# Kernel optimization log

Hardware: AMD Instinct MI355X
Metric: run time of the kernel (lower is better)

Reference implementation:

```python
import jax, jax.numpy as jnp
import numpy as np

# static config (matches init_kwargs / chosen grid)
T, H, W = 8, 32, 32          # video token grid
WT, WH, WW = 4, 8, 8         # swin window
HEADS, HD = 16, 128
DIM = HEADS * HD             # 2048
LT = 256                     # text length
EPS = 1e-6
NT, NH, NW_ = T // WT, H // WH, W // WW
NWIN = NT * NH * NW_
WLEN = WT * WH * WW


def rmsnorm(x, g):
    # x: [..., HD], g: [HD]
    var = jnp.mean(x * x, axis=-1, keepdims=True)
    return x * jax.lax.rsqrt(var + EPS) * g


def setup_inputs() -> dict:
    key = jax.random.key(0)
    ks = jax.random.split(key, 8)
    s = 0.02
    Lv = T * H * W
    return {
        'vid': jax.random.normal(ks[0], (Lv, DIM), jnp.float32),
        'txt': jax.random.normal(ks[1], (LT, DIM), jnp.float32),
        'Wqkv_v': jax.random.normal(ks[2], (DIM, 3 * DIM), jnp.float32) * s,
        'bqkv_v': jnp.zeros((3 * DIM,), jnp.float32),
        'Wqkv_t': jax.random.normal(ks[3], (DIM, 3 * DIM), jnp.float32) * s,
        'bqkv_t': jnp.zeros((3 * DIM,), jnp.float32),
        'Wo_v': jax.random.normal(ks[4], (DIM, DIM), jnp.float32) * s,
        'bo_v': jnp.zeros((DIM,), jnp.float32),
        'Wo_t': jax.random.normal(ks[5], (DIM, DIM), jnp.float32) * s,
        'bo_t': jnp.zeros((DIM,), jnp.float32),
        'gq_v': jnp.ones((HD,), jnp.float32),
        'gk_v': jnp.ones((HD,), jnp.float32),
        'gq_t': jnp.ones((HD,), jnp.float32),
        'gk_t': jnp.ones((HD,), jnp.float32),
    }


def _forward(vid, txt, Wqkv_v, bqkv_v, Wqkv_t, bqkv_t, Wo_v, bo_v, Wo_t, bo_t,
             gq_v, gk_v, gq_t, gk_t):
    # per-modality QKV projections
    vqkv = vid @ Wqkv_v + bqkv_v                      # [Lv, 3*DIM]
    tqkv = txt @ Wqkv_t + bqkv_t                      # [LT, 3*DIM]
    # swin window partition: [T,H,W,C] -> [nWin, WLEN, 3, h, d]
    x = vqkv.reshape(NT, WT, NH, WH, NW_, WW, 3 * DIM)
    x = x.transpose(0, 2, 4, 1, 3, 5, 6).reshape(NWIN, WLEN, 3, HEADS, HD)
    vq, vk, vv = x[:, :, 0], x[:, :, 1], x[:, :, 2]
    t = tqkv.reshape(LT, 3, HEADS, HD)
    tq, tk, tv = t[:, 0], t[:, 1], t[:, 2]
    # QK norm (per-head RMSNorm with affine)
    vq, vk = rmsnorm(vq, gq_v), rmsnorm(vk, gk_v)
    tq, tk = rmsnorm(tq, gq_t), rmsnorm(tk, gk_t)
    # concat full text to every window (repeat_concat_idx)
    bt = lambda a: jnp.broadcast_to(a[None], (NWIN,) + a.shape)
    q = jnp.concatenate([vq, bt(tq)], axis=1)          # [nWin, S, h, d]
    k = jnp.concatenate([vk, bt(tk)], axis=1)
    v = jnp.concatenate([vv, bt(tv)], axis=1)
    # attention within each window (flash-varlen equivalent, equal lengths)
    scale = 1.0 / np.sqrt(HD).astype(np.float32)
    scores = jnp.einsum('nqhd,nkhd->nhqk', q, k) * scale
    p = jax.nn.softmax(scores, axis=-1)
    o = jnp.einsum('nhqk,nkhd->nqhd', p, v)            # [nWin, S, h, d]
    vo = o[:, :WLEN].reshape(NWIN, WLEN, DIM)
    to = o[:, WLEN:].mean(axis=0).reshape(LT, DIM)     # un-repeat text: mean over windows
    # window reverse -> flat [Lv, DIM]
    vo = vo.reshape(NT, NH, NW_, WT, WH, WW, DIM)
    vo = vo.transpose(0, 3, 1, 4, 2, 5, 6).reshape(T * H * W, DIM)
    return (vo @ Wo_v + bo_v, to @ Wo_t + bo_t)


def reference(vid, txt, Wqkv_v, bqkv_v, Wqkv_t, bqkv_t, Wo_v, bo_v, Wo_t, bo_t,
              gq_v, gk_v, gq_t, gk_t):
    return _forward(vid, txt, Wqkv_v, bqkv_v, Wqkv_t, bqkv_t, Wo_v, bo_v,
                    Wo_t, bo_t, gq_v, gk_v, gq_t, gk_t)
```

## Files before the change

### kernel.cpp

```cpp
#include <hip/hip_runtime.h>

typedef unsigned short u16;
typedef unsigned int   u32;
typedef __attribute__((ext_vector_type(8))) short short8;
typedef __attribute__((ext_vector_type(4))) float f32x4;

__device__ __forceinline__ u16 f2bf(float f) {
  union { float f; u32 u; } v; v.f = f;
  u32 r = v.u + 0x7fffu + ((v.u >> 16) & 1u);
  return (u16)(r >> 16);
}
__device__ __forceinline__ float bf2f(u32 bits) {
  union { u32 u; float f; } v; v.u = bits << 16; return v.f;
}
__device__ __forceinline__ void gl_lds16(const u16* g, u16* l) {
  __builtin_amdgcn_global_load_lds(
      (const __attribute__((address_space(1))) void*)g,
      (__attribute__((address_space(3))) void*)l, 16, 0, 0);
}

static constexpr int DIM  = 2048;
static constexpr int NQKV = 6144;

__global__ __launch_bounds__(256) void conv_f32_bf16(const float* __restrict__ in,
                                                     u16* __restrict__ out, int n4) {
  int id = blockIdx.x * 256 + threadIdx.x;
  if (id >= n4) return;
  float4 v = ((const float4*)in)[id];
  u32 lo = (u32)f2bf(v.x) | ((u32)f2bf(v.y) << 16);
  u32 hi = (u32)f2bf(v.z) | ((u32)f2bf(v.w) << 16);
  ((uint2*)out)[id] = make_uint2(lo, hi);
}

__global__ void tconv_kernel(const float* __restrict__ W, u16* __restrict__ Wt, int K, int N) {
  __shared__ float t[32][33];
  int tx = threadIdx.x, ty = threadIdx.y;
  int n0 = blockIdx.x * 32, k0 = blockIdx.y * 32;
  #pragma unroll
  for (int i = 0; i < 4; ++i)
    t[ty + i*8][tx] = W[(size_t)(k0 + ty + i*8) * N + n0 + tx];
  __syncthreads();
  #pragma unroll
  for (int i = 0; i < 4; ++i)
    Wt[(size_t)(n0 + ty + i*8) * K + k0 + tx] = f2bf(t[tx][ty + i*8]);
}

__global__ __launch_bounds__(256) void rms_kernel(u16* __restrict__ x,
                                                  const float* __restrict__ g, int nrows) {
  int w = threadIdx.x >> 6, lane = threadIdx.x & 63;
  int rid = blockIdx.x * 4 + w;
  if (rid >= nrows) return;
  u32* row = (u32*)x + (size_t)rid * 64;
  u32 u = row[lane];
  float f0 = bf2f(u & 0xffffu), f1 = bf2f(u >> 16);
  float s = f0*f0 + f1*f1;
  #pragma unroll
  for (int off = 1; off <= 32; off <<= 1) s += __shfl_xor(s, off);
  float r = rsqrtf(s * (1.0f/128.0f) + 1e-6f);
  float g0 = g[lane*2], g1 = g[lane*2+1];
  row[lane] = (u32)f2bf(f0*r*g0) | ((u32)f2bf(f1*r*g1) << 16);
}

__global__ __launch_bounds__(256)
void vtrans_kernel(const u16* __restrict__ src, u16* __restrict__ dst) {
  __shared__ u16 t[64][130];
  int nh = blockIdx.x, k0 = blockIdx.y * 64;
  const u16* s = src + ((size_t)nh*256 + k0)*128;
  u16* d = dst + (size_t)nh*128*256 + k0;
  int tid = threadIdx.x;
  #pragma unroll
  for (int it = 0; it < 4; ++it) {
    int c = tid + it*256;
    int row = c >> 4, ch = c & 15;
    short8 v = *(const short8*)(s + row*128 + ch*8);
    u32* dst32 = (u32*)&t[row][ch*8];
    const u32* v32 = (const u32*)&v;
    dst32[0] = v32[0]; dst32[1] = v32[1]; dst32[2] = v32[2]; dst32[3] = v32[3];
  }
  __syncthreads();
  #pragma unroll
  for (int it = 0; it < 4; ++it) {
    int c = tid + it*256;
    int dr = c >> 3, kg = c & 7;
    short8 v;
    #pragma unroll
    for (int j = 0; j < 8; ++j) v[j] = (short)t[kg*8+j][dr];
    *(short8*)(d + (size_t)dr*256 + kg*8) = v;
  }
}

template<int EPI>
__global__ __launch_bounds__(512, 2)
void gemm256(const u16* __restrict__ A, const u16* __restrict__ Bt,
             const float* __restrict__ bias,
             u16* __restrict__ o0, u16* __restrict__ o1, u16* __restrict__ o2,
             float* __restrict__ of, int ldo, int M, int N, int K)
{
  __shared__ __align__(16) u16 As[4][256*32];
  __shared__ __align__(16) u16 Bs[4][256*32];
  const int NT = K >> 5;
  int tid = threadIdx.x, lane = tid & 63, w = tid >> 6;
  int l15 = lane & 15, l4 = lane >> 4;
  int wm = w >> 2, wn = w & 3;

  int nbx = gridDim.x;
  int nwg = nbx * gridDim.y;
  int bid = blockIdx.y * nbx + blockIdx.x;
  int cpx = nwg >> 3;
  int swz = (bid & 7) * cpx + (bid >> 3);
  int n0 = (swz % nbx) * 256, m0 = (swz / nbx) * 256;

  int srow = tid >> 2, skc = (tid & 3) ^ ((tid >> 3) & 3);
  const u16* aS = A  + (size_t)(m0 + srow) * K + skc * 8;
  const u16* bS = Bt + (size_t)(n0 + srow) * K + skc * 8;
  const size_t halfStride = 128 * (size_t)K;
  const int ldsBase = w * 512;

  #define STAGE_A(slot, tt, half) \
    gl_lds16(aS + (size_t)(tt)*32 + (half)*halfStride, &As[slot][(half)*4096 + ldsBase])
  #define STAGE_B(slot, tt, half) \
    gl_lds16(bS + (size_t)(tt)*32 + (half)*halfStride, &Bs[slot][(half)*4096 + ldsBase])

  #pragma unroll
  for (int pt = 0; pt < 3; ++pt) {
    STAGE_A(pt, pt, 0); STAGE_A(pt, pt, 1);
    STAGE_B(pt, pt, 0); STAGE_B(pt, pt, 1);
  }

  f32x4 acc[8][4] = {};

  for (int t = 0; t < NT; ++t) {
    if (t < NT - 2)       asm volatile("s_waitcnt vmcnt(8)" ::: "memory");
    else if (t == NT - 2) asm volatile("s_waitcnt vmcnt(4)" ::: "memory");
    else                  asm volatile("s_waitcnt vmcnt(0)" ::: "memory");
    __builtin_amdgcn_s_barrier();
    asm volatile("" ::: "memory");

    const u16* ab = As[t & 3];
    const u16* bb = Bs[t & 3];
    bool st = (t + 3 < NT);
    int slot = (t + 3) & 3;

    short8 bf_[4];
    #pragma unroll
    for (int j = 0; j < 4; ++j) {
      int rb = wn*64 + j*16 + l15;
      bf_[j] = *(const short8*)((const char*)bb + rb*64 + ((l4 ^ ((rb>>1)&3))*16));
    }

    short8 af[4];
    #pragma unroll
    for (int i = 0; i < 4; ++i) {
      int ra = wm*128 + i*16 + l15;
      af[i] = *(const short8*)((const char*)ab + ra*64 + ((l4 ^ ((ra>>1)&3))*16));
    }
    if (st) { STAGE_A(slot, t+3, 0); STAGE_A(slot, t+3, 1); }
    __builtin_amdgcn_s_setprio(1);
    #pragma unroll
    for (int i = 0; i < 4; ++i)
      #pragma unroll
      for (int j = 0; j < 4; ++j)
        acc[i][j] = __builtin_amdgcn_mfma_f32_16x16x32_bf16(af[i], bf_[j], acc[i][j], 0, 0, 0);
    __builtin_amdgcn_s_setprio(0);

    #pragma unroll
    for (int i = 0; i < 4; ++i) {
      int ra = wm*128 + 64 + i*16 + l15;
      af[i] = *(const short8*)((const char*)ab + ra*64 + ((l4 ^ ((ra>>1)&3))*16));
    }
    if (st) { STAGE_B(slot, t+3, 0); STAGE_B(slot, t+3, 1); }
    __builtin_amdgcn_s_setprio(1);
    #pragma unroll
    for (int i = 0; i < 4; ++i)
      #pragma unroll
      for (int j = 0; j < 4; ++j)
        acc[4+i][j] = __builtin_amdgcn_mfma_f32_16x16x32_bf16(af[i], bf_[j], acc[4+i][j], 0, 0, 0);
    __builtin_amdgcn_s_setprio(0);
  }
  #undef STAGE_A
  #undef STAGE_B

  #pragma unroll
  for (int i = 0; i < 8; ++i)
    #pragma unroll
    for (int j = 0; j < 4; ++j)
      #pragma unroll
      for (int r = 0; r < 4; ++r) {
        int m = m0 + wm*128 + i*16 + l4*4 + r;
        int n = n0 + wn*64  + j*16 + l15;
        float v = acc[i][j][r] + bias[n];
        if (EPI == 0) {
          int which = n >> 11, head = (n >> 7) & 15, d = n & 127;
          int t = m >> 10, hh = (m >> 5) & 31, ww = m & 31;
          int win = ((t>>2)<<4) + ((hh>>3)<<2) + (ww>>3);
          int p   = ((t&3)<<6) + ((hh&7)<<3) + (ww&7);
          u16* dst = which == 0 ? o0 : (which == 1 ? o1 : o2);
          dst[((size_t)(win*16 + head)*256 + p)*128 + d] = f2bf(v);
        } else {
          of[(size_t)m * ldo + n] = v;
        }
      }
}

template<int EPI>
__global__ __launch_bounds__(256)
void gemm128(const u16* __restrict__ A, const u16* __restrict__ Bt,
             const float* __restrict__ bias,
             u16* __restrict__ o0, u16* __restrict__ o1, u16* __restrict__ o2,
             float* __restrict__ of, int ldo, int M, int N, int K)
{
  __shared__ __align__(16) u16 As[128*32];
  __shared__ __align__(16) u16 Bs[128*32];
  int tid = threadIdx.x, lane = tid & 63, w = tid >> 6;
  int l15 = lane & 15, l4 = lane >> 4;
  int m0 = blockIdx.y * 128, n0 = blockIdx.x * 128;
  int wr = (w >> 1) * 64, wc = (w & 1) * 64;
  f32x4 acc[4][4] = {};

  int o0b = (w    )*1024 + lane*16;
  int o1b = (w + 4)*1024 + lane*16;
  int r0 = o0b >> 6, c0 = ((o0b >> 4) & 3) ^ ((r0 >> 1) & 3);
  int r1 = o1b >> 6, c1 = ((o1b >> 4) & 3) ^ ((r1 >> 1) & 3);
  const u16* a0 = A  + (size_t)(m0 + r0)*K + c0*8;
  const u16* a1 = A  + (size_t)(m0 + r1)*K + c1*8;
  const u16* b0 = Bt + (size_t)(n0 + r0)*K + c0*8;
  const u16* b1 = Bt + (size_t)(n0 + r1)*K + c1*8;
  u16* dA0 = As + (w    )*512;
  u16* dA1 = As + (w + 4)*512;
  u16* dB0 = Bs + (w    )*512;
  u16* dB1 = Bs + (w + 4)*512;

  for (int k0 = 0; k0 < K; k0 += 32) {
    gl_lds16(a0 + k0, dA0);
    gl_lds16(a1 + k0, dA1);
    gl_lds16(b0 + k0, dB0);
    gl_lds16(b1 + k0, dB1);
    __syncthreads();
    short8 af[4], bfr[4];
    #pragma unroll
    for (int t = 0; t < 4; ++t) {
      int ra = wr + t*16 + l15;
      af[t]  = *(const short8*)((const char*)As + ra*64 + ((l4 ^ ((ra>>1)&3))*16));
      int rb = wc + t*16 + l15;
      bfr[t] = *(const short8*)((const char*)Bs + rb*64 + ((l4 ^ ((rb>>1)&3))*16));
    }
    #pragma unroll
    for (int i = 0; i < 4; ++i)
      #pragma unroll
      for (int j = 0; j < 4; ++j)
        acc[i][j] = __builtin_amdgcn_mfma_f32_16x16x32_bf16(af[i], bfr[j], acc[i][j], 0, 0, 0);
    __syncthreads();
  }

  #pragma unroll
  for (int i = 0; i < 4; ++i)
    #pragma unroll
    for (int j = 0; j < 4; ++j)
      #pragma unroll
      for (int r = 0; r < 4; ++r) {
        int m = m0 + wr + i*16 + l4*4 + r;
        int n = n0 + wc + j*16 + l15;
        float v = acc[i][j][r] + bias[n];
        if (EPI == 1) {
          int which = n >> 11, head = (n >> 7) & 15, d = n & 127;
          u16* dst = which == 0 ? o0 : (which == 1 ? o1 : o2);
          dst[((size_t)head*256 + m)*128 + d] = f2bf(v);
        } else {
          of[(size_t)m * ldo + n] = v;
        }
      }
}

__global__ __launch_bounds__(512)
void attn_kernel(const u16* __restrict__ vq, const u16* __restrict__ vk, const u16* __restrict__ vv,
                 const u16* __restrict__ tq, const u16* __restrict__ tk, const u16* __restrict__ tv,
                 const float* __restrict__ gq_v, const float* __restrict__ gq_t,
                 u16* __restrict__ vo, float* __restrict__ to_acc)
{
  __shared__ __align__(16) u16 Ks[64*128];
  __shared__ __align__(16) u16 Vt[128*64];
  __shared__ __align__(16) u16 Ps[8][16*80];
  int tid = threadIdx.x, lane = tid & 63, w = tid >> 6;
  int l15 = lane & 15, l4 = lane >> 4;
  int nh_ = blockIdx.x;
  int h = nh_ & 15;
  int n = nh_ >> 4;
  int qt = blockIdx.y * 128 + w * 16;

  const u16* Qb; const float* gq;
  if (qt < 256) { Qb = vq + ((size_t)nh_*256 + qt)*128; gq = gq_v; }
  else          { Qb = tq + ((size_t)h  *256 + (qt-256))*128; gq = gq_t; }
  short8 qf[4];
  float qv[4][8];
  float ss = 0.f;
  #pragma unroll
  for (int dt = 0; dt < 4; ++dt) {
    qf[dt] = *(const short8*)(Qb + l15*128 + l4*8 + dt*32);
    #pragma unroll
    for (int j = 0; j < 8; ++j) {
      float f = bf2f((u16)qf[dt][j]);
      qv[dt][j] = f; ss += f*f;
    }
  }
  ss += __shfl_xor(ss, 16); ss += __shfl_xor(ss, 32);
  float rr = rsqrtf(ss * (1.0f/128.0f) + 1e-6f);
  #pragma unroll
  for (int dt = 0; dt < 4; ++dt) {
    float4 g0 = *(const float4*)(gq + l4*8 + dt*32);
    float4 g1 = *(const float4*)(gq + l4*8 + dt*32 + 4);
    qf[dt][0] = (short)f2bf(qv[dt][0]*rr*g0.x); qf[dt][1] = (short)f2bf(qv[dt][1]*rr*g0.y);
    qf[dt][2] = (short)f2bf(qv[dt][2]*rr*g0.z); qf[dt][3] = (short)f2bf(qv[dt][3]*rr*g0.w);
    qf[dt][4] = (short)f2bf(qv[dt][4]*rr*g1.x); qf[dt][5] = (short)f2bf(qv[dt][5]*rr*g1.y);
    qf[dt][6] = (short)f2bf(qv[dt][6]*rr*g1.z); qf[dt][7] = (short)f2bf(qv[dt][7]*rr*g1.w);
  }

  int oK0 = w*1024 + lane*16, oK1 = oK0 + 8192;
  int kr0 = oK0 >> 8, kc0 = ((oK0 >> 4) & 15) ^ (kr0 & 7);
  int kr1 = oK1 >> 8, kc1 = ((oK1 >> 4) & 15) ^ (kr1 & 7);
  int vd0 = oK0 >> 7, vc0 = ((oK0 >> 4) & 7) ^ (vd0 & 7);
  int vd1 = oK1 >> 7, vc1 = ((oK1 >> 4) & 7) ^ (vd1 & 7);
  u16* KD0 = Ks + (w*1024)/2;  u16* KD1 = Ks + (w*1024 + 8192)/2;
  u16* VD0 = Vt + (w*1024)/2;  u16* VD1 = Vt + (w*1024 + 8192)/2;

  f32x4 o_[8] = {};
  float m_run[4] = {-1e30f,-1e30f,-1e30f,-1e30f};
  float l_run[4] = {0.f,0.f,0.f,0.f};
  const float scale = 0.08838834764831845f;

  for (int c = 0; c < 8; ++c) {
    int kb = c * 64;
    const u16* Kc; const u16* Vb; int vkb;
    if (kb < 256) { Kc = vk + ((size_t)nh_*256 + kb)*128; Vb = vv + (size_t)nh_*128*256; vkb = kb; }
    else          { Kc = tk + ((size_t)h  *256 + (kb-256))*128; Vb = tv + (size_t)h*128*256; vkb = kb - 256; }
    gl_lds16(Kc + kr0*128 + kc0*8, KD0);
    gl_lds16(Kc + kr1*128 + kc1*8, KD1);
    gl_lds16(Vb + (size_t)vd0*256 + vkb + vc0*8, VD0);
    gl_lds16(Vb + (size_t)vd1*256 + vkb + vc1*8, VD1);
    __syncthreads();

    f32x4 s4[4];
    #pragma unroll
    for (int kt = 0; kt < 4; ++kt) {
      f32x4 sa = {0.f,0.f,0.f,0.f};
      int key = kt*16 + l15;
      #pragma unroll
      for (int dt = 0; dt < 4; ++dt) {
        int c16b = l4 + dt*4;
        short8 kf = *(const short8*)((const char*)Ks + key*256 + (((c16b ^ (key&7)))*16));
        sa = __builtin_amdgcn_mfma_f32_16x16x32_bf16(qf[dt], kf, sa, 0, 0, 0);
      }
      s4[kt] = sa;
    }

    float f_[4];
    #pragma unroll
    for (int r = 0; r < 4; ++r) {
      float mx = fmaxf(fmaxf(s4[0][r], s4[1][r]), fmaxf(s4[2][r], s4[3][r])) * scale;
      #pragma unroll
      for (int off = 1; off <= 8; off <<= 1) mx = fmaxf(mx, __shfl_xor(mx, off));
      float nm = fmaxf(m_run[r], mx);
      f_[r] = __expf(m_run[r] - nm);
      m_run[r] = nm;
    }
    float p[4][4];
    #pragma unroll
    for (int kt = 0; kt < 4; ++kt)
      #pragma unroll
      for (int r = 0; r < 4; ++r)
        p[kt][r] = __expf(s4[kt][r]*scale - m_run[r]);
    #pragma unroll
    for (int r = 0; r < 4; ++r) {
      float sum = p[0][r] + p[1][r] + p[2][r] + p[3][r];
      #pragma unroll
      for (int off = 1; off <= 8; off <<= 1) sum += __shfl_xor(sum, off);
      l_run[r] = l_run[r]*f_[r] + sum;
    }
    #pragma unroll
    for (int dt = 0; dt < 8; ++dt) {
      f32x4 t = o_[dt];
      t[0]*=f_[0]; t[1]*=f_[1]; t[2]*=f_[2]; t[3]*=f_[3];
      o_[dt] = t;
    }

    u16* pb = Ps[w];
    #pragma unroll
    for (int kt = 0; kt < 4; ++kt)
      #pragma unroll
      for (int r = 0; r < 4; ++r)
        pb[(l4*4 + r)*80 + kt*16 + l15] = f2bf(p[kt][r]);
    __syncthreads();
    #pragma unroll
    for (int ks = 0; ks < 2; ++ks) {
      short8 pa = *(const short8*)((const char*)pb + l15*160 + ks*64 + l4*16);
      #pragma unroll
      for (int dt = 0; dt < 8; ++dt) {
        int d = dt*16 + l15;
        short8 vf = *(const short8*)((const char*)Vt + d*128 + (((ks*4 + l4) ^ (d&7))<<4));
        o_[dt] = __builtin_amdgcn_mfma_f32_16x16x32_bf16(pa, vf, o_[dt], 0, 0, 0);
      }
    }
    __syncthreads();
  }

  float inv[4];
  #pragma unroll
  for (int r = 0; r < 4; ++r) inv[r] = 1.0f / l_run[r];
  int nt = n >> 4, nh2 = (n >> 2) & 3, nw = n & 3;
  #pragma unroll
  for (int dt = 0; dt < 8; ++dt) {
    int d = dt*16 + l15;
    int col = h*128 + d;
    #pragma unroll
    for (int r = 0; r < 4; ++r) {
      float val = o_[dt][r] * inv[r];
      int q = qt + l4*4 + r;
      if (q < 256) {
        int wt = q >> 6, wh = (q >> 3) & 7, ww = q & 7;
        int rg = ((nt*4 + wt)*32 + (nh2*8 + wh))*32 + (nw*8 + ww);
        vo[(size_t)rg*2048 + col] = f2bf(val);
      } else {
        atomicAdd(to_acc + (size_t)(q - 256)*2048 + col, val * (1.0f/32.0f));
      }
    }
  }
}

extern "C" void kernel_launch(void* const* d_in, const int* in_sizes, int n_in,
                              void* d_out, int out_size, void* d_ws, size_t ws_size,
                              hipStream_t stream) {
  const float* vid    = (const float*)d_in[0];
  const float* txt    = (const float*)d_in[1];
  const float* Wqkv_v = (const float*)d_in[2];
  const float* bqkv_v = (const float*)d_in[3];
  const float* Wqkv_t = (const float*)d_in[4];
  const float* bqkv_t = (const float*)d_in[5];
  const float* Wo_v   = (const float*)d_in[6];
  const float* bo_v   = (const float*)d_in[7];
  const float* Wo_t   = (const float*)d_in[8];
  const float* bo_t   = (const float*)d_in[9];
  const float* gq_v   = (const float*)d_in[10];
  const float* gk_v   = (const float*)d_in[11];
  const float* gq_t   = (const float*)d_in[12];
  const float* gk_t   = (const float*)d_in[13];
  float* out = (float*)d_out;

  char* p = (char*)d_ws;
  u16* vid_bf   = (u16*)p;  p += 8192ull*2048*2;
  u16* txt_bf   = (u16*)p;  p += 256ull*2048*2;
  u16* Wqkv_v_t = (u16*)p;  p += 6144ull*2048*2;
  u16* Wqkv_t_t = (u16*)p;  p += 6144ull*2048*2;
  u16* Wo_v_t   = (u16*)p;  p += 2048ull*2048*2;
  u16* Wo_t_t   = (u16*)p;  p += 2048ull*2048*2;
  u16* vq_w     = (u16*)p;  p += 32ull*16*256*128*2;
  u16* vk_w     = (u16*)p;  p += 32ull*16*256*128*2;
  u16* vv_w     = (u16*)p;  p += 32ull*16*256*128*2;
  u16* tq_w     = (u16*)p;  p += 16ull*256*128*2;
  u16* tk_w     = (u16*)p;  p += 16ull*256*128*2;
  u16* tv_w     = (u16*)p;  p += 16ull*256*128*2;
  u16* vo_pre   = (u16*)p;  p += 8192ull*2048*2;
  float* to_pre = (float*)p; p += 256ull*2048*4;
  u16* to_bf    = (u16*)p;  p += 256ull*2048*2;
  u16* vvT = vid_bf;
  u16* tvT = vid_bf + 512ull*128*256;

  hipMemsetAsync(to_pre, 0, 256ull*2048*4, stream);

  conv_f32_bf16<<<dim3(16384), dim3(256), 0, stream>>>(vid, vid_bf, 8192*2048/4);
  conv_f32_bf16<<<dim3(512),   dim3(256), 0, stream>>>(txt, txt_bf, 256*2048/4);
  tconv_kernel<<<dim3(192,64), dim3(32,8), 0, stream>>>(Wqkv_v, Wqkv_v_t, 2048, 6144);
  tconv_kernel<<<dim3(192,64), dim3(32,8), 0, stream>>>(Wqkv_t, Wqkv_t_t, 2048, 6144);
  tconv_kernel<<<dim3(64,64),  dim3(32,8), 0, stream>>>(Wo_v,   Wo_v_t,   2048, 2048);
  tconv_kernel<<<dim3(64,64),  dim3(32,8), 0, stream>>>(Wo_t,   Wo_t_t,   2048, 2048);

  gemm256<0><<<dim3(24,32), dim3(512), 0, stream>>>(vid_bf, Wqkv_v_t, bqkv_v,
      vq_w, vk_w, vv_w, nullptr, 0, 8192, NQKV, DIM);
  gemm128<1><<<dim3(48,2),  dim3(256), 0, stream>>>(txt_bf, Wqkv_t_t, bqkv_t,
      tq_w, tk_w, tv_w, nullptr, 0, 256, NQKV, DIM);

  vtrans_kernel<<<dim3(512,4), dim3(256), 0, stream>>>(vv_w, vvT);
  vtrans_kernel<<<dim3(16,4),  dim3(256), 0, stream>>>(tv_w, tvT);

  rms_kernel<<<dim3(32768), dim3(256), 0, stream>>>(vk_w, gk_v, 32*16*256);
  rms_kernel<<<dim3(1024),  dim3(256), 0, stream>>>(tk_w, gk_t, 16*256);

  attn_kernel<<<dim3(512,4), dim3(512), 0, stream>>>(vq_w, vk_w, vvT, tq_w, tk_w, tvT,
                                                     gq_v, gq_t, vo_pre, to_pre);

  conv_f32_bf16<<<dim3(512), dim3(256), 0, stream>>>(to_pre, to_bf, 256*2048/4);

  gemm256<2><<<dim3(8,32), dim3(512), 0, stream>>>(vo_pre, Wo_v_t, bo_v,
      nullptr, nullptr, nullptr, out, 2048, 8192, 2048, 2048);
  gemm128<2><<<dim3(16,2), dim3(256), 0, stream>>>(to_bf, Wo_t_t, bo_t,
      nullptr, nullptr, nullptr, out + 16777216, 2048, 256, 2048, 2048);
}
```

Before: 641.8 us.

## Restructure GEMM barrier schedule and remap attention blocks with priority hints

```diff
diff --git a/kernel.cpp b/kernel.cpp
--- a/kernel.cpp
+++ b/kernel.cpp
@@ -126,35 +126,32 @@
     STAGE_A(pt, pt, 0); STAGE_A(pt, pt, 1);
     STAGE_B(pt, pt, 0); STAGE_B(pt, pt, 1);
   }
+  asm volatile("s_waitcnt vmcnt(8)" ::: "memory");
+  __builtin_amdgcn_s_barrier();
 
   f32x4 acc[8][4] = {};
 
   for (int t = 0; t < NT; ++t) {
-    if (t < NT - 2)       asm volatile("s_waitcnt vmcnt(8)" ::: "memory");
-    else if (t == NT - 2) asm volatile("s_waitcnt vmcnt(4)" ::: "memory");
-    else                  asm volatile("s_waitcnt vmcnt(0)" ::: "memory");
-    __builtin_amdgcn_s_barrier();
-    asm volatile("" ::: "memory");
-
     const u16* ab = As[t & 3];
     const u16* bb = Bs[t & 3];
     bool st = (t + 3 < NT);
     int slot = (t + 3) & 3;
 
-    short8 bf_[4];
+    short8 bf_[4], af[4];
     #pragma unroll
     for (int j = 0; j < 4; ++j) {
       int rb = wn*64 + j*16 + l15;
       bf_[j] = *(const short8*)((const char*)bb + rb*64 + ((l4 ^ ((rb>>1)&3))*16));
     }
-
-    short8 af[4];
     #pragma unroll
     for (int i = 0; i < 4; ++i) {
       int ra = wm*128 + i*16 + l15;
       af[i] = *(const short8*)((const char*)ab + ra*64 + ((l4 ^ ((ra>>1)&3))*16));
     }
     if (st) { STAGE_A(slot, t+3, 0); STAGE_A(slot, t+3, 1); }
+    __builtin_amdgcn_s_barrier();
+    asm volatile("s_waitcnt lgkmcnt(0)" ::: "memory");
+    __builtin_amdgcn_sched_barrier(0);
     __builtin_amdgcn_s_setprio(1);
     #pragma unroll
     for (int i = 0; i < 4; ++i)
@@ -162,6 +159,7 @@
       for (int j = 0; j < 4; ++j)
         acc[i][j] = __builtin_amdgcn_mfma_f32_16x16x32_bf16(af[i], bf_[j], acc[i][j], 0, 0, 0);
     __builtin_amdgcn_s_setprio(0);
+    __builtin_amdgcn_s_barrier();
 
     #pragma unroll
     for (int i = 0; i < 4; ++i) {
@@ -169,6 +167,9 @@
       af[i] = *(const short8*)((const char*)ab + ra*64 + ((l4 ^ ((ra>>1)&3))*16));
     }
     if (st) { STAGE_B(slot, t+3, 0); STAGE_B(slot, t+3, 1); }
+    __builtin_amdgcn_s_barrier();
+    asm volatile("s_waitcnt lgkmcnt(0)" ::: "memory");
+    __builtin_amdgcn_sched_barrier(0);
     __builtin_amdgcn_s_setprio(1);
     #pragma unroll
     for (int i = 0; i < 4; ++i)
@@ -176,6 +177,10 @@
       for (int j = 0; j < 4; ++j)
         acc[4+i][j] = __builtin_amdgcn_mfma_f32_16x16x32_bf16(af[i], bf_[j], acc[4+i][j], 0, 0, 0);
     __builtin_amdgcn_s_setprio(0);
+    if (t <= NT - 4)      asm volatile("s_waitcnt vmcnt(8)" ::: "memory");
+    else if (t == NT - 3) asm volatile("s_waitcnt vmcnt(4)" ::: "memory");
+    else if (t == NT - 2) asm volatile("s_waitcnt vmcnt(0)" ::: "memory");
+    __builtin_amdgcn_s_barrier();
   }
   #undef STAGE_A
   #undef STAGE_B
@@ -282,10 +287,12 @@
   __shared__ __align__(16) u16 Ps[8][16*80];
   int tid = threadIdx.x, lane = tid & 63, w = tid >> 6;
   int l15 = lane & 15, l4 = lane >> 4;
-  int nh_ = blockIdx.x;
+  int bid = blockIdx.x;
+  int logical = (bid & 7) * 256 + (bid >> 3);
+  int nh_ = logical >> 2, qq = logical & 3;
   int h = nh_ & 15;
   int n = nh_ >> 4;
-  int qt = blockIdx.y * 128 + w * 16;
+  int qt = qq * 128 + w * 16;
 
   const u16* Qb; const float* gq;
   if (qt < 256) { Qb = vq + ((size_t)nh_*256 + qt)*128; gq = gq_v; }
@@ -326,6 +333,7 @@
   float m_run[4] = {-1e30f,-1e30f,-1e30f,-1e30f};
   float l_run[4] = {0.f,0.f,0.f,0.f};
   const float scale = 0.08838834764831845f;
+  u16* pb = Ps[w];
 
   for (int c = 0; c < 8; ++c) {
     int kb = c * 64;
@@ -339,6 +347,7 @@
     __syncthreads();
 
     f32x4 s4[4];
+    __builtin_amdgcn_s_setprio(1);
     #pragma unroll
     for (int kt = 0; kt < 4; ++kt) {
       f32x4 sa = {0.f,0.f,0.f,0.f};
@@ -351,6 +360,7 @@
       }
       s4[kt] = sa;
     }
+    __builtin_amdgcn_s_setprio(0);
 
     float f_[4];
     #pragma unroll
@@ -382,22 +392,22 @@
       o_[dt] = t;
     }
 
-    u16* pb = Ps[w];
     #pragma unroll
     for (int kt = 0; kt < 4; ++kt)
       #pragma unroll
       for (int r = 0; r < 4; ++r)
         pb[(l4*4 + r)*80 + kt*16 + l15] = f2bf(p[kt][r]);
-    __syncthreads();
     #pragma unroll
     for (int ks = 0; ks < 2; ++ks) {
       short8 pa = *(const short8*)((const char*)pb + l15*160 + ks*64 + l4*16);
+      __builtin_amdgcn_s_setprio(1);
       #pragma unroll
       for (int dt = 0; dt < 8; ++dt) {
         int d = dt*16 + l15;
         short8 vf = *(const short8*)((const char*)Vt + d*128 + (((ks*4 + l4) ^ (d&7))<<4));
         o_[dt] = __builtin_amdgcn_mfma_f32_16x16x32_bf16(pa, vf, o_[dt], 0, 0, 0);
       }
+      __builtin_amdgcn_s_setprio(0);
     }
     __syncthreads();
   }
@@ -483,8 +493,8 @@
   rms_kernel<<<dim3(32768), dim3(256), 0, stream>>>(vk_w, gk_v, 32*16*256);
   rms_kernel<<<dim3(1024),  dim3(256), 0, stream>>>(tk_w, gk_t, 16*256);
 
-  attn_kernel<<<dim3(512,4), dim3(512), 0, stream>>>(vq_w, vk_w, vvT, tq_w, tk_w, tvT,
-                                                     gq_v, gq_t, vo_pre, to_pre);
+  attn_kernel<<<dim3(2048), dim3(512), 0, stream>>>(vq_w, vk_w, vvT, tq_w, tk_w, tvT,
+                                                    gq_v, gq_t, vo_pre, to_pre);
 
   conv_f32_bf16<<<dim3(512), dim3(256), 0, stream>>>(to_pre, to_bf, 256*2048/4);
 
```

New measurement: 639.4 us. No clear change (-0.4%).
